# Performance work log

Hardware: AMD Instinct MI355X
Metric: run time of the kernel (lower is better)

The kernel has to match this reference:

```python
import jax, jax.numpy as jnp
import numpy as np

N_NODES = 100000
DROPOUT_P = 0.2


def _gcn_conv(x, W, b, src, dst, n_nodes):
    # PyG GCNConv: h = x @ W; add self-loops; sym-norm deg^-1/2 aggregation; + bias
    h = x @ W  # [N, D_out]
    loops = jnp.arange(n_nodes, dtype=src.dtype)
    src_all = jnp.concatenate([src, loops])
    dst_all = jnp.concatenate([dst, loops])
    deg = jax.ops.segment_sum(jnp.ones_like(dst_all, dtype=h.dtype), dst_all,
                              num_segments=n_nodes)  # includes self-loops
    dinv = jnp.where(deg > 0, jax.lax.rsqrt(deg), 0.0)
    norm = dinv[src_all] * dinv[dst_all]  # [E+N]
    msg = h[src_all] * norm[:, None]      # gather + scale
    out = jax.ops.segment_sum(msg, dst_all, num_segments=n_nodes)  # scatter-add
    return out + b


def setup_inputs() -> dict:
    key = jax.random.key(0)
    k1, k2, k3, k4 = jax.random.split(key, 4)
    x = jax.random.normal(k1, (N_NODES, 128), dtype=jnp.float32)
    edge_index = jax.random.randint(k2, (2, 1600000), 0, N_NODES, dtype=jnp.int64)
    W1 = jax.random.normal(k3, (128, 64), dtype=jnp.float32) * (1.0 / np.sqrt(128))
    b1 = jnp.zeros((64,), dtype=jnp.float32)
    W2 = jax.random.normal(k4, (64, 32), dtype=jnp.float32) * (1.0 / np.sqrt(64))
    b2 = jnp.zeros((32,), dtype=jnp.float32)
    return {"x": x, "edge_index": edge_index, "W1": W1, "b1": b1, "W2": W2, "b2": b2}


def reference(x, edge_index, W1, b1, W2, b2):
    src, dst = edge_index[0], edge_index[1]
    h1 = _gcn_conv(x, W1, b1, src, dst, N_NODES)
    h1 = jax.nn.relu(h1)
    # F.dropout defaults to training=True -> apply inverted dropout with fixed key
    keep = jax.random.bernoulli(jax.random.key(42), 1.0 - DROPOUT_P, h1.shape)
    h1 = jnp.where(keep, h1 / (1.0 - DROPOUT_P), 0.0)
    h2 = _gcn_conv(h1, W2, b2, src, dst, N_NODES)
    return h2
```

## Files before the change

### kernel.cpp

```cpp
#include <hip/hip_runtime.h>
#include <stdint.h>

#define DIN 128
#define D1 64
#define D2 32
#define MAXDEG 48
#define BCAP 4608
#define CBLK 8192

__device__ __forceinline__ unsigned short f2bf(float v) {
  unsigned u = __float_as_uint(v);
  unsigned r = u + 0x7fffu + ((u >> 16) & 1u);
  return (unsigned short)(r >> 16);
}
__device__ __forceinline__ float bf2f(unsigned short b) {
  return __uint_as_float(((unsigned)b) << 16);
}

__device__ __forceinline__ float node_dinv(const int* __restrict__ deg, int n) {
  return (float)(1.0 / sqrt((double)(deg[n] + 1)));
}

__device__ __forceinline__ unsigned rotl32(unsigned x, int r) {
  return (x << r) | (x >> (32 - r));
}

__device__ __forceinline__ unsigned threefry_fold(unsigned ctr) {
  unsigned k0 = 0u, k1 = 42u;
  unsigned ks0 = k0, ks1 = k1, ks2 = k0 ^ k1 ^ 0x1BD11BDAu;
  unsigned x0 = 0u, x1 = ctr;
  x0 += ks0; x1 += ks1;
#define TF_ROUND(r) { x0 += x1; x1 = rotl32(x1, (r)); x1 ^= x0; }
  TF_ROUND(13) TF_ROUND(15) TF_ROUND(26) TF_ROUND(6)
  x0 += ks1; x1 += ks2 + 1u;
  TF_ROUND(17) TF_ROUND(29) TF_ROUND(16) TF_ROUND(24)
  x0 += ks2; x1 += ks0 + 2u;
  TF_ROUND(13) TF_ROUND(15) TF_ROUND(26) TF_ROUND(6)
  x0 += ks0; x1 += ks1 + 3u;
  TF_ROUND(17) TF_ROUND(29) TF_ROUND(16) TF_ROUND(24)
  x0 += ks1; x1 += ks2 + 4u;
  TF_ROUND(13) TF_ROUND(15) TF_ROUND(26) TF_ROUND(6)
  x0 += ks2; x1 += ks0 + 5u;
#undef TF_ROUND
  return x0 ^ x1;
}

__device__ __forceinline__ float dropout_scale(unsigned idx) {
  unsigned bits = threefry_fold(idx);
  float u = __uint_as_float((bits >> 9) | 0x3f800000u) - 1.0f;
  return (u < 0.8f) ? 1.25f : 0.0f;
}

__global__ __launch_bounds__(256) void bin_kernel(const int* __restrict__ src,
                                                  const int* __restrict__ dst,
                                                  int* __restrict__ cursor,
                                                  uint2* __restrict__ binned,
                                                  int E, int NBK) {
  __shared__ int cnt[512];
  __shared__ int cbase[512];
  const int tid = threadIdx.x;
  const int e0 = blockIdx.x * CBLK;

  for (int b = tid; b < NBK; b += 256) cnt[b] = 0;
  __syncthreads();

#pragma unroll 4
  for (int i = 0; i < CBLK / 256; i++) {
    int e = e0 + tid + 256 * i;
    if (e < E) atomicAdd(&cnt[dst[e] >> 8], 1);
  }
  __syncthreads();

  for (int b = tid; b < NBK; b += 256) {
    int c = cnt[b];
    if (c > 0) cbase[b] = b * BCAP + atomicAdd(&cursor[b], c);
    cnt[b] = 0;
  }
  __syncthreads();

#pragma unroll 4
  for (int i = 0; i < CBLK / 256; i++) {
    int e = e0 + tid + 256 * i;
    if (e < E) {
      int d = dst[e];
      int b = d >> 8;
      int rk = atomicAdd(&cnt[b], 1);
      int pos = cbase[b] + rk;
      if (pos - b * BCAP < BCAP)
        binned[pos] = make_uint2((unsigned)d, (unsigned)src[e]);
    }
  }
}

__global__ __launch_bounds__(256) void ellbuild_kernel(const uint2* __restrict__ binned,
                                                       const int* __restrict__ cursor,
                                                       int* __restrict__ deg,
                                                       int* __restrict__ ell, int N) {
  __shared__ int r[256];
  const int tid = threadIdx.x;
  const int b = blockIdx.x;
  const int nodebase = b << 8;
  r[tid] = 0;
  __syncthreads();

  int cnt = cursor[b];
  if (cnt > BCAP) cnt = BCAP;
  const uint2* seg = binned + (size_t)b * BCAP;
  for (int i = tid; i < cnt; i += 256) {
    uint2 p = seg[i];
    int local = (int)p.x - nodebase;
    int rk = atomicAdd(&r[local], 1);
    if (rk < MAXDEG) ell[(int)p.x * MAXDEG + rk] = (int)p.y;
  }
  __syncthreads();

  int node = nodebase + tid;
  if (node < N) deg[node] = r[tid];
}

__global__ __launch_bounds__(256) void gemm1_kernel(const float* __restrict__ x,
                                                    const float* __restrict__ W1,
                                                    const int* __restrict__ deg,
                                                    unsigned short* __restrict__ h1p, int N) {
  __shared__ float xT[32][65];
  __shared__ float Wl[32][D1];
  const int tid = threadIdx.x;
  const int rowbase = blockIdx.x * 64;
  const int tx = tid & 15;
  const int ty = tid >> 4;
  float acc[4][4];
#pragma unroll
  for (int i = 0; i < 4; i++)
#pragma unroll
    for (int j = 0; j < 4; j++) acc[i][j] = 0.f;

  for (int c4 = 0; c4 < 4; c4++) {
    const int k0 = c4 * 32;
#pragma unroll
    for (int i = 0; i < 2; i++) {
      int f = tid + 256 * i;
      int row = f >> 3;
      int kq = (f & 7) * 4;
      int gr = rowbase + row;
      float4 vv = make_float4(0.f, 0.f, 0.f, 0.f);
      if (gr < N) vv = *(const float4*)(x + (size_t)gr * DIN + k0 + kq);
      xT[kq + 0][row] = vv.x;
      xT[kq + 1][row] = vv.y;
      xT[kq + 2][row] = vv.z;
      xT[kq + 3][row] = vv.w;
    }
#pragma unroll
    for (int i = 0; i < 2; i++) {
      int f = tid + 256 * i;
      int k = f >> 4;
      int cc = (f & 15) * 4;
      *(float4*)&Wl[k][cc] = *(const float4*)(W1 + (size_t)(k0 + k) * D1 + cc);
    }
    __syncthreads();
#pragma unroll 4
    for (int k = 0; k < 32; k++) {
      float4 a = *(const float4*)&xT[k][4 * ty];
      float4 b = *(const float4*)&Wl[k][4 * tx];
      float av[4] = {a.x, a.y, a.z, a.w};
      float bv[4] = {b.x, b.y, b.z, b.w};
#pragma unroll
      for (int i = 0; i < 4; i++)
#pragma unroll
        for (int j = 0; j < 4; j++) acc[i][j] = fmaf(av[i], bv[j], acc[i][j]);
    }
    __syncthreads();
  }

#pragma unroll
  for (int i = 0; i < 4; i++) {
    int gr = rowbase + 4 * ty + i;
    if (gr < N) {
      float di = node_dinv(deg, gr);
      ushort4 o;
      o.x = f2bf(acc[i][0] * di);
      o.y = f2bf(acc[i][1] * di);
      o.z = f2bf(acc[i][2] * di);
      o.w = f2bf(acc[i][3] * di);
      *(ushort4*)(h1p + (size_t)gr * D1 + 4 * tx) = o;
    }
  }
}

__global__ __launch_bounds__(256) void agg1_kernel(const int* __restrict__ deg,
                                                   const int* __restrict__ ell,
                                                   const unsigned short* __restrict__ h1p,
                                                   const float* __restrict__ b1,
                                                   float* __restrict__ h1d, int N) {
  const int wslot = __builtin_amdgcn_readfirstlane(threadIdx.x >> 6);
  const int d = blockIdx.x * 4 + wslot;
  const int f = threadIdx.x & 63;
  const int cnt = min(deg[d], MAXDEG);
  const int base = d * MAXDEG;
  float acc = bf2f(h1p[(size_t)d * D1 + f]);
  int j = 0;
  for (; j + 7 < cnt; j += 8) {
    int s[8];
#pragma unroll
    for (int i = 0; i < 8; i++) s[i] = ell[base + j + i];
    unsigned short a[8];
#pragma unroll
    for (int i = 0; i < 8; i++) a[i] = h1p[(size_t)s[i] * D1 + f];
#pragma unroll
    for (int i = 0; i < 8; i++) acc += bf2f(a[i]);
  }
  for (; j < cnt; ++j) acc += bf2f(h1p[(size_t)ell[base + j] * D1 + f]);
  float di = node_dinv(deg, d);
  float v = fmaf(di, acc, b1[f]);
  v = fmaxf(v, 0.0f);
  v *= dropout_scale((unsigned)(d * D1 + f));
  h1d[(size_t)d * D1 + f] = v;
}

__global__ __launch_bounds__(256) void gemm2_kernel(const float* __restrict__ h1d,
                                                    const float* __restrict__ W2,
                                                    const int* __restrict__ deg,
                                                    unsigned short* __restrict__ h2p, int N) {
  __shared__ float hT[D1][129];
  __shared__ float Wl[D1][D2];
  const int tid = threadIdx.x;
  const int rowbase = blockIdx.x * 128;

#pragma unroll
  for (int i = 0; i < 8; i++) {
    int f = tid + 256 * i;
    int row = f >> 4;
    int kq = (f & 15) * 4;
    int gr = rowbase + row;
    float4 v = make_float4(0.f, 0.f, 0.f, 0.f);
    if (gr < N) v = *(const float4*)(h1d + (size_t)gr * D1 + kq);
    hT[kq + 0][row] = v.x;
    hT[kq + 1][row] = v.y;
    hT[kq + 2][row] = v.z;
    hT[kq + 3][row] = v.w;
  }
#pragma unroll
  for (int i = 0; i < 2; i++) {
    int f = tid + 256 * i;
    int k = f >> 3;
    int c = (f & 7) * 4;
    *(float4*)&Wl[k][c] = *(const float4*)(W2 + (size_t)k * D2 + c);
  }
  __syncthreads();

  const int tx = tid & 7;
  const int ty = tid >> 3;
  float acc[4][4];
#pragma unroll
  for (int i = 0; i < 4; i++)
#pragma unroll
    for (int j = 0; j < 4; j++) acc[i][j] = 0.f;

#pragma unroll 4
  for (int k = 0; k < D1; k++) {
    float4 a = *(const float4*)&hT[k][4 * ty];
    float4 b = *(const float4*)&Wl[k][4 * tx];
    float av[4] = {a.x, a.y, a.z, a.w};
    float bv[4] = {b.x, b.y, b.z, b.w};
#pragma unroll
    for (int i = 0; i < 4; i++)
#pragma unroll
      for (int j = 0; j < 4; j++) acc[i][j] = fmaf(av[i], bv[j], acc[i][j]);
  }

#pragma unroll
  for (int i = 0; i < 4; i++) {
    int gr = rowbase + 4 * ty + i;
    if (gr < N) {
      float di = node_dinv(deg, gr);
      ushort4 o;
      o.x = f2bf(acc[i][0] * di);
      o.y = f2bf(acc[i][1] * di);
      o.z = f2bf(acc[i][2] * di);
      o.w = f2bf(acc[i][3] * di);
      *(ushort4*)(h2p + (size_t)gr * D2 + 4 * tx) = o;
    }
  }
}

__global__ __launch_bounds__(256) void agg2_kernel(const int* __restrict__ deg,
                                                   const int* __restrict__ ell,
                                                   const unsigned short* __restrict__ h2p,
                                                   const float* __restrict__ b2,
                                                   float* __restrict__ out, int N) {
  const int wslot = __builtin_amdgcn_readfirstlane(threadIdx.x >> 6);
  const int d = blockIdx.x * 4 + wslot;
  const int lane = threadIdx.x & 63;
  const int f = lane & 31;
  const int h = lane >> 5;
  const int cnt = min(deg[d], MAXDEG);
  const int base = d * MAXDEG;
  float acc = (h == 0) ? bf2f(h2p[(size_t)d * D2 + f]) : 0.0f;
  int j = h;
  for (; j + 6 < cnt; j += 8) {
    int s0 = ell[base + j], s1 = ell[base + j + 2];
    int s2 = ell[base + j + 4], s3 = ell[base + j + 6];
    unsigned short a0 = h2p[(size_t)s0 * D2 + f];
    unsigned short a1 = h2p[(size_t)s1 * D2 + f];
    unsigned short a2 = h2p[(size_t)s2 * D2 + f];
    unsigned short a3 = h2p[(size_t)s3 * D2 + f];
    acc += bf2f(a0); acc += bf2f(a1); acc += bf2f(a2); acc += bf2f(a3);
  }
  for (; j < cnt; j += 2) acc += bf2f(h2p[(size_t)ell[base + j] * D2 + f]);
  acc += __shfl_down(acc, 32, 64);
  if (h == 0) {
    out[(size_t)d * D2 + f] = fmaf(node_dinv(deg, d), acc, b2[f]);
  }
}

extern "C" void kernel_launch(void* const* d_in, const int* in_sizes, int n_in,
                              void* d_out, int out_size, void* d_ws, size_t ws_size,
                              hipStream_t stream) {
  const float* x  = (const float*)d_in[0];
  const int*   ei = (const int*)d_in[1];
  const float* W1 = (const float*)d_in[2];
  const float* b1 = (const float*)d_in[3];
  const float* W2 = (const float*)d_in[4];
  const float* b2 = (const float*)d_in[5];
  const int N = in_sizes[0] / DIN;
  const int E = in_sizes[1] / 2;
  const int NBK = (N + 255) >> 8;
  const int* src = ei;
  const int* dst = ei + E;
  float* out = (float*)d_out;

  char* ws = (char*)d_ws;
  size_t off = 0;
  auto alloc = [&](size_t bytes) -> char* {
    char* p = ws + off;
    off += (bytes + 255) / 256 * 256;
    return p;
  };
  unsigned short* h1p = (unsigned short*)alloc((size_t)N * D1 * 2);
  float*          h1d = (float*)alloc((size_t)N * D1 * 4);
  int*            ell = (int*)alloc((size_t)N * MAXDEG * 4);
  int*            deg = (int*)alloc((size_t)N * 4);
  int*         cursor = (int*)alloc((size_t)NBK * 4);
  unsigned short* h2p = h1p;
  uint2*       binned = (uint2*)h1d;
  (void)ws_size; (void)n_in; (void)out_size;

  hipMemsetAsync(cursor, 0, (size_t)NBK * 4, stream);

  bin_kernel<<<(E + CBLK - 1) / CBLK, 256, 0, stream>>>(src, dst, cursor, binned, E, NBK);
  ellbuild_kernel<<<NBK, 256, 0, stream>>>(binned, cursor, deg, ell, N);
  gemm1_kernel<<<(N + 63) / 64, 256, 0, stream>>>(x, W1, deg, h1p, N);
  agg1_kernel<<<N / 4, 256, 0, stream>>>(deg, ell, h1p, b1, h1d, N);
  gemm2_kernel<<<(N + 127) / 128, 256, 0, stream>>>(h1d, W2, deg, h2p, N);
  agg2_kernel<<<N / 4, 256, 0, stream>>>(deg, ell, h2p, b2, out, N);
}
```

Baseline: 298.8 us.

## Vectorize neighbor gathers in aggregation kernels with 16-byte loads and LDS reduction

Both aggregation kernels now split each wave across several edges at once, with each lane fetching 8 bf16 features (16 bytes) per neighbor instead of one 2-byte value. Partial sums go through shared memory and are reduced per feature. The aim is fewer, wider memory transactions and more gathers in flight. Separately, deg^-1/2 is precomputed once in the ELL build kernel, removing the repeated double-precision sqrt in the GEMM and aggregation kernels. The cost is extra shared-memory traffic for the reduction, plus masked tail handling that reads ELL slots past cnt (the ELL buffer is padded for this).

Result: faster. 255.4 us (-14.5%).

```diff
diff --git a/kernel.cpp b/kernel.cpp
--- a/kernel.cpp
+++ b/kernel.cpp
@@ -13,13 +13,8 @@
   unsigned r = u + 0x7fffu + ((u >> 16) & 1u);
   return (unsigned short)(r >> 16);
 }
-__device__ __forceinline__ float bf2f(unsigned short b) {
-  return __uint_as_float(((unsigned)b) << 16);
-}
-
-__device__ __forceinline__ float node_dinv(const int* __restrict__ deg, int n) {
-  return (float)(1.0 / sqrt((double)(deg[n] + 1)));
-}
+__device__ __forceinline__ float bflo(unsigned u) { return __uint_as_float(u << 16); }
+__device__ __forceinline__ float bfhi(unsigned u) { return __uint_as_float(u & 0xffff0000u); }
 
 __device__ __forceinline__ unsigned rotl32(unsigned x, int r) {
   return (x << r) | (x >> (32 - r));
@@ -51,6 +46,22 @@
   return (u < 0.8f) ? 1.25f : 0.0f;
 }
 
+__device__ __forceinline__ uint4 grow64(const unsigned short* p, int s, int fc) {
+  return *(const uint4*)((const char*)p + (((unsigned)s << 7) + ((unsigned)fc << 1)));
+}
+__device__ __forceinline__ uint4 grow32(const unsigned short* p, int s, int fc) {
+  return *(const uint4*)((const char*)p + (((unsigned)s << 6) + ((unsigned)fc << 1)));
+}
+
+__device__ __forceinline__ void addpk(float2& a, unsigned u) {
+  a.x += bflo(u);
+  a.y += bfhi(u);
+}
+__device__ __forceinline__ void addpkm(float2& a, unsigned u, float m) {
+  a.x = fmaf(m, bflo(u), a.x);
+  a.y = fmaf(m, bfhi(u), a.y);
+}
+
 __global__ __launch_bounds__(256) void bin_kernel(const int* __restrict__ src,
                                                   const int* __restrict__ dst,
                                                   int* __restrict__ cursor,
@@ -95,6 +106,7 @@
 __global__ __launch_bounds__(256) void ellbuild_kernel(const uint2* __restrict__ binned,
                                                        const int* __restrict__ cursor,
                                                        int* __restrict__ deg,
+                                                       float* __restrict__ dinv,
                                                        int* __restrict__ ell, int N) {
   __shared__ int r[256];
   const int tid = threadIdx.x;
@@ -115,12 +127,16 @@
   __syncthreads();
 
   int node = nodebase + tid;
-  if (node < N) deg[node] = r[tid];
+  if (node < N) {
+    int dg = r[tid];
+    deg[node] = dg;
+    dinv[node] = (float)(1.0 / sqrt((double)(dg + 1)));
+  }
 }
 
 __global__ __launch_bounds__(256) void gemm1_kernel(const float* __restrict__ x,
                                                     const float* __restrict__ W1,
-                                                    const int* __restrict__ deg,
+                                                    const float* __restrict__ dinv,
                                                     unsigned short* __restrict__ h1p, int N) {
   __shared__ float xT[32][65];
   __shared__ float Wl[32][D1];
@@ -175,7 +191,7 @@
   for (int i = 0; i < 4; i++) {
     int gr = rowbase + 4 * ty + i;
     if (gr < N) {
-      float di = node_dinv(deg, gr);
+      float di = dinv[gr];
       ushort4 o;
       o.x = f2bf(acc[i][0] * di);
       o.y = f2bf(acc[i][1] * di);
@@ -187,38 +203,71 @@
 }
 
 __global__ __launch_bounds__(256) void agg1_kernel(const int* __restrict__ deg,
+                                                   const float* __restrict__ dinv,
                                                    const int* __restrict__ ell,
                                                    const unsigned short* __restrict__ h1p,
                                                    const float* __restrict__ b1,
                                                    float* __restrict__ h1d, int N) {
+  __shared__ float red[4][512];
   const int wslot = __builtin_amdgcn_readfirstlane(threadIdx.x >> 6);
   const int d = blockIdx.x * 4 + wslot;
-  const int f = threadIdx.x & 63;
+  const int lane = threadIdx.x & 63;
+  const int eslot = lane >> 3;
+  const int fc = (lane & 7) << 3;
   const int cnt = min(deg[d], MAXDEG);
   const int base = d * MAXDEG;
-  float acc = bf2f(h1p[(size_t)d * D1 + f]);
+
+  float2 acc[4];
+  {
+    uint4 sv = grow64(h1p, d, fc);
+    float m = (eslot == 0) ? 1.0f : 0.0f;
+    acc[0] = make_float2(m * bflo(sv.x), m * bfhi(sv.x));
+    acc[1] = make_float2(m * bflo(sv.y), m * bfhi(sv.y));
+    acc[2] = make_float2(m * bflo(sv.z), m * bfhi(sv.z));
+    acc[3] = make_float2(m * bflo(sv.w), m * bfhi(sv.w));
+  }
+
   int j = 0;
-  for (; j + 7 < cnt; j += 8) {
-    int s[8];
-#pragma unroll
-    for (int i = 0; i < 8; i++) s[i] = ell[base + j + i];
-    unsigned short a[8];
-#pragma unroll
-    for (int i = 0; i < 8; i++) a[i] = h1p[(size_t)s[i] * D1 + f];
-#pragma unroll
-    for (int i = 0; i < 8; i++) acc += bf2f(a[i]);
-  }
-  for (; j < cnt; ++j) acc += bf2f(h1p[(size_t)ell[base + j] * D1 + f]);
-  float di = node_dinv(deg, d);
-  float v = fmaf(di, acc, b1[f]);
-  v = fmaxf(v, 0.0f);
-  v *= dropout_scale((unsigned)(d * D1 + f));
-  h1d[(size_t)d * D1 + f] = v;
+  for (; j + 16 <= cnt; j += 16) {
+    int s0 = ell[base + j + eslot];
+    int s1 = ell[base + j + 8 + eslot];
+    uint4 v0 = grow64(h1p, s0, fc);
+    uint4 v1 = grow64(h1p, s1, fc);
+    addpk(acc[0], v0.x); addpk(acc[1], v0.y); addpk(acc[2], v0.z); addpk(acc[3], v0.w);
+    addpk(acc[0], v1.x); addpk(acc[1], v1.y); addpk(acc[2], v1.z); addpk(acc[3], v1.w);
+  }
+  if (j < cnt) {
+    int e0 = j + eslot;
+    int e1 = e0 + 8;
+    int s0 = ell[base + e0];
+    int s1 = ell[base + e1];
+    s0 = (e0 < cnt) ? s0 : d;
+    s1 = (e1 < cnt) ? s1 : d;
+    float m0 = (e0 < cnt) ? 1.0f : 0.0f;
+    float m1 = (e1 < cnt) ? 1.0f : 0.0f;
+    uint4 v0 = grow64(h1p, s0, fc);
+    uint4 v1 = grow64(h1p, s1, fc);
+    addpkm(acc[0], v0.x, m0); addpkm(acc[1], v0.y, m0); addpkm(acc[2], v0.z, m0); addpkm(acc[3], v0.w, m0);
+    addpkm(acc[0], v1.x, m1); addpkm(acc[1], v1.y, m1); addpkm(acc[2], v1.z, m1); addpkm(acc[3], v1.w, m1);
+  }
+
+  float* wred = red[wslot];
+  *(float4*)&wred[eslot * 64 + fc]     = make_float4(acc[0].x, acc[0].y, acc[1].x, acc[1].y);
+  *(float4*)&wred[eslot * 64 + fc + 4] = make_float4(acc[2].x, acc[2].y, acc[3].x, acc[3].y);
+  const int f = fc + eslot;
+  float v = 0.f;
+#pragma unroll
+  for (int e = 0; e < 8; e++) v += wred[e * 64 + f];
+
+  float o = fmaf(dinv[d], v, b1[f]);
+  o = fmaxf(o, 0.0f);
+  o *= dropout_scale((unsigned)(d * D1 + f));
+  h1d[(size_t)d * D1 + f] = o;
 }
 
 __global__ __launch_bounds__(256) void gemm2_kernel(const float* __restrict__ h1d,
                                                     const float* __restrict__ W2,
-                                                    const int* __restrict__ deg,
+                                                    const float* __restrict__ dinv,
                                                     unsigned short* __restrict__ h2p, int N) {
   __shared__ float hT[D1][129];
   __shared__ float Wl[D1][D2];
@@ -271,7 +320,7 @@
   for (int i = 0; i < 4; i++) {
     int gr = rowbase + 4 * ty + i;
     if (gr < N) {
-      float di = node_dinv(deg, gr);
+      float di = dinv[gr];
       ushort4 o;
       o.x = f2bf(acc[i][0] * di);
       o.y = f2bf(acc[i][1] * di);
@@ -283,32 +332,57 @@
 }
 
 __global__ __launch_bounds__(256) void agg2_kernel(const int* __restrict__ deg,
+                                                   const float* __restrict__ dinv,
                                                    const int* __restrict__ ell,
                                                    const unsigned short* __restrict__ h2p,
                                                    const float* __restrict__ b2,
                                                    float* __restrict__ out, int N) {
+  __shared__ float red[4][512];
   const int wslot = __builtin_amdgcn_readfirstlane(threadIdx.x >> 6);
   const int d = blockIdx.x * 4 + wslot;
   const int lane = threadIdx.x & 63;
-  const int f = lane & 31;
-  const int h = lane >> 5;
+  const int eslot = lane >> 2;
+  const int fc = (lane & 3) << 3;
   const int cnt = min(deg[d], MAXDEG);
   const int base = d * MAXDEG;
-  float acc = (h == 0) ? bf2f(h2p[(size_t)d * D2 + f]) : 0.0f;
-  int j = h;
-  for (; j + 6 < cnt; j += 8) {
-    int s0 = ell[base + j], s1 = ell[base + j + 2];
-    int s2 = ell[base + j + 4], s3 = ell[base + j + 6];
-    unsigned short a0 = h2p[(size_t)s0 * D2 + f];
-    unsigned short a1 = h2p[(size_t)s1 * D2 + f];
-    unsigned short a2 = h2p[(size_t)s2 * D2 + f];
-    unsigned short a3 = h2p[(size_t)s3 * D2 + f];
-    acc += bf2f(a0); acc += bf2f(a1); acc += bf2f(a2); acc += bf2f(a3);
-  }
-  for (; j < cnt; j += 2) acc += bf2f(h2p[(size_t)ell[base + j] * D2 + f]);
-  acc += __shfl_down(acc, 32, 64);
-  if (h == 0) {
-    out[(size_t)d * D2 + f] = fmaf(node_dinv(deg, d), acc, b2[f]);
+
+  float2 acc[4];
+  {
+    uint4 sv = grow32(h2p, d, fc);
+    float m = (eslot == 0) ? 1.0f : 0.0f;
+    acc[0] = make_float2(m * bflo(sv.x), m * bfhi(sv.x));
+    acc[1] = make_float2(m * bflo(sv.y), m * bfhi(sv.y));
+    acc[2] = make_float2(m * bflo(sv.z), m * bfhi(sv.z));
+    acc[3] = make_float2(m * bflo(sv.w), m * bfhi(sv.w));
+  }
+
+  int j = 0;
+  for (; j + 16 <= cnt; j += 16) {
+    int s = ell[base + j + eslot];
+    uint4 v = grow32(h2p, s, fc);
+    addpk(acc[0], v.x); addpk(acc[1], v.y); addpk(acc[2], v.z); addpk(acc[3], v.w);
+  }
+  if (j < cnt) {
+    int e = j + eslot;
+    int s = ell[base + e];
+    s = (e < cnt) ? s : d;
+    float m = (e < cnt) ? 1.0f : 0.0f;
+    uint4 v = grow32(h2p, s, fc);
+    addpkm(acc[0], v.x, m); addpkm(acc[1], v.y, m); addpkm(acc[2], v.z, m); addpkm(acc[3], v.w, m);
+  }
+
+  float* wred = red[wslot];
+  *(float4*)&wred[eslot * 32 + fc]     = make_float4(acc[0].x, acc[0].y, acc[1].x, acc[1].y);
+  *(float4*)&wred[eslot * 32 + fc + 4] = make_float4(acc[2].x, acc[2].y, acc[3].x, acc[3].y);
+  const int f = fc + (eslot & 7);
+  const int ebase = (lane >= 32) ? 8 : 0;
+  float v = 0.f;
+#pragma unroll
+  for (int e = 0; e < 8; e++) v += wred[(ebase + e) * 32 + f];
+  v += __shfl_down(v, 32, 64);
+
+  if (lane < 32) {
+    out[(size_t)d * D2 + f] = fmaf(dinv[d], v, b2[f]);
   }
 }
 
@@ -337,8 +411,9 @@
   };
   unsigned short* h1p = (unsigned short*)alloc((size_t)N * D1 * 2);
   float*          h1d = (float*)alloc((size_t)N * D1 * 4);
-  int*            ell = (int*)alloc((size_t)N * MAXDEG * 4);
+  int*            ell = (int*)alloc(((size_t)N * MAXDEG + 64) * 4);
   int*            deg = (int*)alloc((size_t)N * 4);
+  float*        dinvp = (float*)alloc((size_t)N * 4);
   int*         cursor = (int*)alloc((size_t)NBK * 4);
   unsigned short* h2p = h1p;
   uint2*       binned = (uint2*)h1d;
@@ -347,9 +422,9 @@
   hipMemsetAsync(cursor, 0, (size_t)NBK * 4, stream);
 
   bin_kernel<<<(E + CBLK - 1) / CBLK, 256, 0, stream>>>(src, dst, cursor, binned, E, NBK);
-  ellbuild_kernel<<<NBK, 256, 0, stream>>>(binned, cursor, deg, ell, N);
-  gemm1_kernel<<<(N + 63) / 64, 256, 0, stream>>>(x, W1, deg, h1p, N);
-  agg1_kernel<<<N / 4, 256, 0, stream>>>(deg, ell, h1p, b1, h1d, N);
-  gemm2_kernel<<<(N + 127) / 128, 256, 0, stream>>>(h1d, W2, deg, h2p, N);
-  agg2_kernel<<<N / 4, 256, 0, stream>>>(deg, ell, h2p, b2, out, N);
-}
+  ellbuild_kernel<<<NBK, 256, 0, stream>>>(binned, cursor, deg, dinvp, ell, N);
+  gemm1_kernel<<<(N + 63) / 64, 256, 0, stream>>>(x, W1, dinvp, h1p, N);
+  agg1_kernel<<<N / 4, 256, 0, stream>>>(deg, dinvp, ell, h1p, b1, h1d, N);
+  gemm2_kernel<<<(N + 127) / 128, 256, 0, stream>>>(h1d, W2, dinvp, h2p, N);
+  agg2_kernel<<<N / 4, 256, 0, stream>>>(deg, dinvp, ell, h2p, b2, out, N);
+}
```
